# Kernel tuning notes

Hardware: AMD Instinct MI355X
Metric: run time of the kernel (lower is better)

Reference implementation:

```python
import jax, jax.numpy as jnp
import numpy as np

EMB = 384
NH = 6
HD = EMB // NH
EPS = 1e-5


def _ln(x, w, b):
    m = jnp.mean(x, axis=-1, keepdims=True)
    v = jnp.mean((x - m) ** 2, axis=-1, keepdims=True)
    return (x - m) * jax.lax.rsqrt(v + EPS) * w + b


def setup_inputs() -> dict:
    key = jax.random.key(0)
    ks = jax.random.split(key, 24)
    s = 0.02
    d = {
        "x": jax.random.normal(ks[0], (4, 4096, EMB), jnp.float32),
        "cond": jax.random.normal(ks[1], (4, EMB), jnp.float32),
        # AdaLN projections (weight stored as (in,out), bias (out,))
        "g1_w": jax.random.normal(ks[2], (EMB, EMB)) * s, "g1_b": jnp.zeros((EMB,)),
        "be1_w": jax.random.normal(ks[3], (EMB, EMB)) * s, "be1_b": jnp.zeros((EMB,)),
        "a1_w": jax.random.normal(ks[4], (EMB, EMB)) * s, "a1_b": jnp.zeros((EMB,)),
        "g2_w": jax.random.normal(ks[5], (EMB, EMB)) * s, "g2_b": jnp.zeros((EMB,)),
        "be2_w": jax.random.normal(ks[6], (EMB, EMB)) * s, "be2_b": jnp.zeros((EMB,)),
        "a2_w": jax.random.normal(ks[7], (EMB, EMB)) * s, "a2_b": jnp.zeros((EMB,)),
        "ln1_w": jnp.ones((EMB,)), "ln1_b": jnp.zeros((EMB,)),
        "ln2_w": jnp.ones((EMB,)), "ln2_b": jnp.zeros((EMB,)),
        "wq": jax.random.normal(ks[8], (EMB, EMB)) * s,
        "wk": jax.random.normal(ks[9], (EMB, EMB)) * s,
        "wv": jax.random.normal(ks[10], (EMB, EMB)) * s,
        "wo": jax.random.normal(ks[11], (EMB, EMB)) * s,
        "ff1_w": jax.random.normal(ks[12], (EMB, 4 * EMB)) * s, "ff1_b": jnp.zeros((4 * EMB,)),
        "ff2_w": jax.random.normal(ks[13], (4 * EMB, EMB)) * s, "ff2_b": jnp.zeros((EMB,)),
    }
    return d


def reference(x, cond,
              g1_w, g1_b, be1_w, be1_b, a1_w, a1_b,
              g2_w, g2_b, be2_w, be2_b, a2_w, a2_b,
              ln1_w, ln1_b, ln2_w, ln2_b,
              wq, wk, wv, wo,
              ff1_w, ff1_b, ff2_w, ff2_b):
    B, S, E = x.shape
    # AdaLN conditioning projections: (B, E)
    gamma1 = cond @ g1_w + g1_b
    beta1 = cond @ be1_w + be1_b
    alpha1 = cond @ a1_w + a1_b
    gamma2 = cond @ g2_w + g2_b
    beta2 = cond @ be2_w + be2_b
    alpha2 = cond @ a2_w + a2_b

    # Attention branch with AdaLN modulation
    y = _ln(x, ln1_w, ln1_b)
    y = y * (1.0 + gamma1[:, None, :]) + beta1[:, None, :]
    q = (y @ wq).reshape(B, S, NH, HD)
    k = (y @ wk).reshape(B, S, NH, HD)
    v = (y @ wv).reshape(B, S, NH, HD)
    scale = 1.0 / jnp.sqrt(jnp.array(HD, x.dtype))
    attn = jnp.einsum('bqhd,bkhd->bhqk', q, k) * scale  # [B,H,S,S]
    attn = jax.nn.softmax(attn, axis=-1)
    y = jnp.einsum('bhqk,bkhd->bqhd', attn, v).reshape(B, S, E)
    y = (y @ wo) * alpha1[:, None, :]
    y = x + y

    # FFN branch with AdaLN modulation
    z = _ln(y, ln2_w, ln2_b)
    z = z * (1.0 + gamma2[:, None, :]) + beta2[:, None, :]
    z = jax.nn.relu(z @ ff1_w + ff1_b) @ ff2_w + ff2_b
    z = z * alpha2[:, None, :]
    return y + z
```

## Files before the change

kernel.cpp:

```cpp
#include <hip/hip_runtime.h>
#include <stdint.h>

#define E 384
#define SEQ 4096
#define BATCH 4
#define NHEAD 6
#define HD 64
#define M_TOK 16384
#define QKVN 1152
#define FFH 1536

typedef __bf16 bf16x8 __attribute__((ext_vector_type(8)));
typedef __bf16 bf16x4 __attribute__((ext_vector_type(4)));
typedef float floatx4 __attribute__((ext_vector_type(4)));
typedef unsigned int uintx2 __attribute__((ext_vector_type(2)));
typedef unsigned int uintx4 __attribute__((ext_vector_type(4)));

__device__ __forceinline__ unsigned short f2b(float f) {
  unsigned int u = __builtin_bit_cast(unsigned int, f);
  u += 0x7fffu + ((u >> 16) & 1u);
  return (unsigned short)(u >> 16);
}

__device__ __forceinline__ void gl_lds16(const void* g, void* l) {
  __builtin_amdgcn_global_load_lds((__attribute__((address_space(1))) void*)g,
                                   (__attribute__((address_space(3))) void*)l,
                                   16, 0, 0);
}

__device__ __forceinline__ floatx4 mfma16(bf16x8 a, bf16x8 b, floatx4 c) {
  return __builtin_amdgcn_mfma_f32_16x16x32_bf16(a, b, c, 0, 0, 0);
}

__global__ __launch_bounds__(256) void prep_weights(
    const float* __restrict__ wq, const float* __restrict__ wk,
    const float* __restrict__ wv, const float* __restrict__ wo,
    const float* __restrict__ f1, const float* __restrict__ f2,
    unsigned short* __restrict__ qkv_t, unsigned short* __restrict__ wo_t,
    unsigned short* __restrict__ f1_t, unsigned short* __restrict__ f2_t) {
  int tid = blockIdx.x * 256 + threadIdx.x;
  const int R0 = QKVN * E;
  const int R1 = E * E;
  const int R2 = FFH * E;
  if (tid < R0) {
    int n = tid / E, k = tid - n * E;
    float v = (n < E) ? wq[k * E + n] : (n < 2 * E) ? wk[k * E + n - E] : wv[k * E + n - 2 * E];
    qkv_t[tid] = f2b(v);
  } else if (tid < R0 + R1) {
    int id = tid - R0;
    int n = id / E, k = id - n * E;
    wo_t[id] = f2b(wo[k * E + n]);
  } else if (tid < R0 + R1 + R2) {
    int id = tid - (R0 + R1);
    int n = id / E, k = id - n * E;
    f1_t[id] = f2b(f1[k * FFH + n]);
  } else {
    int id = tid - (R0 + R1 + R2);
    int n = id / FFH, k = id - n * FFH;
    f2_t[id] = f2b(f2[k * E + n]);
  }
}

__global__ __launch_bounds__(256) void cond_proj(
    const float* __restrict__ cond,
    const float* __restrict__ w0, const float* __restrict__ b0,
    const float* __restrict__ w1, const float* __restrict__ b1,
    const float* __restrict__ w2, const float* __restrict__ b2,
    const float* __restrict__ w3, const float* __restrict__ b3,
    const float* __restrict__ w4, const float* __restrict__ b4,
    const float* __restrict__ w5, const float* __restrict__ b5,
    float* __restrict__ outp) {
  int tid = blockIdx.x * 256 + threadIdx.x;
  int j = tid / (BATCH * E);
  int rem = tid - j * (BATCH * E);
  int b = rem / E, o = rem - b * E;
  const float* w; const float* bb;
  switch (j) {
    case 0: w = w0; bb = b0; break;
    case 1: w = w1; bb = b1; break;
    case 2: w = w2; bb = b2; break;
    case 3: w = w3; bb = b3; break;
    case 4: w = w4; bb = b4; break;
    default: w = w5; bb = b5; break;
  }
  float acc = bb[o];
  const float* c = cond + b * E;
  for (int i = 0; i < E; i++) acc += c[i] * w[i * E + o];
  outp[tid] = acc;
}

__global__ __launch_bounds__(256) void ln_mod(
    const float* __restrict__ in, const float* __restrict__ lw,
    const float* __restrict__ lb, const float* __restrict__ gamma,
    const float* __restrict__ beta, unsigned short* __restrict__ outb) {
  int lane = threadIdx.x & 63, wave = threadIdx.x >> 6;
  int m = blockIdx.x * 4 + wave;
  int b = m >> 12;
  const float* row = in + (size_t)m * E;
  float v[6], s = 0.f, s2 = 0.f;
#pragma unroll
  for (int i = 0; i < 6; i++) {
    float xv = row[lane + i * 64];
    v[i] = xv; s += xv; s2 += xv * xv;
  }
#pragma unroll
  for (int off = 32; off; off >>= 1) {
    s += __shfl_xor(s, off, 64);
    s2 += __shfl_xor(s2, off, 64);
  }
  float mean = s * (1.f / E);
  float var = s2 * (1.f / E) - mean * mean;
  float inv = rsqrtf(var + 1e-5f);
#pragma unroll
  for (int i = 0; i < 6; i++) {
    int e = lane + i * 64;
    float y = (v[i] - mean) * inv * lw[e] + lb[e];
    float g = gamma[b * E + e], be = beta[b * E + e];
    outb[(size_t)m * E + e] = f2b(y * (1.f + g) + be);
  }
}

template <int EPI>
__global__ __launch_bounds__(256) void gemm_bt(
    const unsigned short* __restrict__ A, const unsigned short* __restrict__ Bt,
    const float* __restrict__ bias, const float* __restrict__ alpha,
    const float* __restrict__ resid, float* __restrict__ outf,
    unsigned short* __restrict__ outb, int N, int K) {
  __shared__ __align__(16) unsigned short As[128 * 32];
  __shared__ __align__(16) unsigned short Bs[128 * 32];
  int t = threadIdx.x, lane = t & 63, wave = t >> 6;
  int m0 = blockIdx.y * 128, n0 = blockIdx.x * 128;
  int m15 = lane & 15, quad = lane >> 4;

  floatx4 acc[4][4];
  floatx4 vz = {0.f, 0.f, 0.f, 0.f};
#pragma unroll
  for (int i = 0; i < 4; i++)
#pragma unroll
    for (int j = 0; j < 4; j++) acc[i][j] = vz;

  int wm = (wave >> 1) * 64, wn = (wave & 1) * 64;
  int gsw = (quad ^ (m15 & 3)) * 8;

  for (int k0 = 0; k0 < K; k0 += 32) {
#pragma unroll
    for (int c = 0; c < 2; c++) {
      int t2 = c * 256 + t;
      int r = t2 >> 2;
      int G = (t2 & 3) ^ (r & 3);
      gl_lds16(A + (size_t)(m0 + r) * K + k0 + G * 8, As + (size_t)(c * 256 + wave * 64) * 8);
      gl_lds16(Bt + (size_t)(n0 + r) * K + k0 + G * 8, Bs + (size_t)(c * 256 + wave * 64) * 8);
    }
    __syncthreads();
    bf16x8 af[4], bf[4];
#pragma unroll
    for (int i = 0; i < 4; i++) {
      af[i] = *(const bf16x8*)&As[(wm + i * 16 + m15) * 32 + gsw];
      bf[i] = *(const bf16x8*)&Bs[(wn + i * 16 + m15) * 32 + gsw];
    }
#pragma unroll
    for (int mi = 0; mi < 4; mi++)
#pragma unroll
      for (int ni = 0; ni < 4; ni++) acc[mi][ni] = mfma16(af[mi], bf[ni], acc[mi][ni]);
    __syncthreads();
  }

  int rbase = quad * 4;
#pragma unroll
  for (int mi = 0; mi < 4; mi++) {
#pragma unroll
    for (int ni = 0; ni < 4; ni++) {
#pragma unroll
      for (int r = 0; r < 4; r++) {
        int row = m0 + wm + mi * 16 + rbase + r;
        int col = n0 + wn + ni * 16 + m15;
        float v = acc[mi][ni][r];
        if (EPI == 0) {
          outb[(size_t)row * N + col] = f2b(v);
        } else if (EPI == 1) {
          int b = row >> 12;
          size_t o = (size_t)row * E + col;
          outf[o] = resid[o] + v * alpha[b * E + col];
        } else if (EPI == 2) {
          v += bias[col];
          outb[(size_t)row * N + col] = f2b(v > 0.f ? v : 0.f);
        } else {
          int b = row >> 12;
          size_t o = (size_t)row * E + col;
          outf[o] = outf[o] + (v + bias[col]) * alpha[b * E + col];
        }
      }
    }
  }
}

template <int EPI>
__global__ __launch_bounds__(256) void gemm64(
    const unsigned short* __restrict__ A, const unsigned short* __restrict__ Bt,
    const float* __restrict__ bias, const float* __restrict__ alpha,
    const float* __restrict__ resid, float* __restrict__ outf,
    unsigned short* __restrict__ outb, int N, int K) {
  __shared__ __align__(16) unsigned short As[64 * 32];
  __shared__ __align__(16) unsigned short Bs[128 * 32];
  int t = threadIdx.x, lane = t & 63, wave = t >> 6;
  int m0 = blockIdx.y * 64, n0 = blockIdx.x * 128;
  int m15 = lane & 15, quad = lane >> 4;

  floatx4 acc[4][2];
  floatx4 vz = {0.f, 0.f, 0.f, 0.f};
#pragma unroll
  for (int i = 0; i < 4; i++)
#pragma unroll
    for (int j = 0; j < 2; j++) acc[i][j] = vz;

  int wn = wave * 32;
  int gsw = (quad ^ (m15 & 3)) * 8;

  for (int k0 = 0; k0 < K; k0 += 32) {
    {
      int r = t >> 2;
      int G = (t & 3) ^ (r & 3);
      gl_lds16(A + (size_t)(m0 + r) * K + k0 + G * 8, As + (size_t)(wave * 64) * 8);
    }
#pragma unroll
    for (int c = 0; c < 2; c++) {
      int t2 = c * 256 + t;
      int r = t2 >> 2;
      int G = (t2 & 3) ^ (r & 3);
      gl_lds16(Bt + (size_t)(n0 + r) * K + k0 + G * 8, Bs + (size_t)(c * 256 + wave * 64) * 8);
    }
    __syncthreads();
    bf16x8 af[4], bf[2];
#pragma unroll
    for (int i = 0; i < 4; i++) af[i] = *(const bf16x8*)&As[(i * 16 + m15) * 32 + gsw];
#pragma unroll
    for (int j = 0; j < 2; j++) bf[j] = *(const bf16x8*)&Bs[(wn + j * 16 + m15) * 32 + gsw];
#pragma unroll
    for (int mi = 0; mi < 4; mi++)
#pragma unroll
      for (int ni = 0; ni < 2; ni++) acc[mi][ni] = mfma16(af[mi], bf[ni], acc[mi][ni]);
    __syncthreads();
  }

  int rbase = quad * 4;
#pragma unroll
  for (int mi = 0; mi < 4; mi++) {
#pragma unroll
    for (int ni = 0; ni < 2; ni++) {
#pragma unroll
      for (int r = 0; r < 4; r++) {
        int row = m0 + mi * 16 + rbase + r;
        int col = n0 + wn + ni * 16 + m15;
        float v = acc[mi][ni][r];
        if (EPI == 1) {
          int b = row >> 12;
          size_t o = (size_t)row * E + col;
          outf[o] = resid[o] + v * alpha[b * E + col];
        } else {
          int b = row >> 12;
          size_t o = (size_t)row * E + col;
          outf[o] = outf[o] + (v + bias[col]) * alpha[b * E + col];
        }
      }
    }
  }
}

__global__ __launch_bounds__(256) void flash_attn(const unsigned short* __restrict__ qkv,
                                                  unsigned short* __restrict__ outb) {
  __shared__ __align__(16) unsigned short Qs[128 * 64];
  __shared__ __align__(16) unsigned short Ks[2][64 * 64];
  __shared__ __align__(16) unsigned short Vt[2][64 * 64];
  int t = threadIdx.x, lane = t & 63, wave = t >> 6;
  int m15 = lane & 15, quad = lane >> 4;
  int q0 = blockIdx.x * 128;
  int bh = blockIdx.y;
  int b = bh / NHEAD, h = bh - b * NHEAD;
  const unsigned short* qp = qkv + (size_t)b * SEQ * QKVN + h * HD;
  const unsigned short* kp = qp + E;
  const unsigned short* vp = qp + 2 * E;
  int kpr = t & 31, dg = t >> 5;

#pragma unroll
  for (int c = 0; c < 4; c++) {
    int slot = c * 256 + t;
    int qr = slot >> 3, s = slot & 7;
    int g = s ^ (qr & 7);
    gl_lds16(qp + (size_t)(q0 + qr) * QKVN + g * 8, Qs + (size_t)(c * 256 + wave * 64) * 8);
  }

  auto stageK = [&](int kb0, unsigned short* Kbuf) {
#pragma unroll
    for (int c = 0; c < 2; c++) {
      int slot = c * 256 + t;
      int kr = slot >> 3, s = slot & 7;
      int g = s ^ (kr & 7);
      gl_lds16(kp + (size_t)(kb0 + kr) * QKVN + g * 8, Kbuf + (size_t)(c * 256 + wave * 64) * 8);
    }
  };
  auto loadV = [&](int kb0, int4& r0, int4& r1) {
    r0 = *(const int4*)(vp + (size_t)(kb0 + 2 * kpr) * QKVN + dg * 8);
    r1 = *(const int4*)(vp + (size_t)(kb0 + 2 * kpr + 1) * QKVN + dg * 8);
  };
  auto writeVt = [&](unsigned short* Vbuf, int4 r0, int4 r1) {
    const unsigned short* u0 = (const unsigned short*)&r0;
    const unsigned short* u1 = (const unsigned short*)&r1;
    int kg = kpr >> 2, pos = kpr & 3;
    unsigned int* V32 = (unsigned int*)Vbuf;
#pragma unroll
    for (int i = 0; i < 8; i++) {
      int d = dg * 8 + i;
      V32[d * 32 + ((kg ^ i ^ dg) & 7) * 4 + pos] =
          (unsigned int)u0[i] | ((unsigned int)u1[i] << 16);
    }
  };

  stageK(0, Ks[0]);
  int4 va, vb;
  loadV(0, va, vb);
  writeVt(Vt[0], va, vb);
  __syncthreads();

  const float QSCALE = 0.125f * 1.44269504f;
  bf16x8 qf[2][2];
#pragma unroll
  for (int mt = 0; mt < 2; mt++) {
    int qr = wave * 32 + mt * 16 + m15;
#pragma unroll
    for (int dh = 0; dh < 2; dh++) {
      bf16x8 v = *(const bf16x8*)&Qs[qr * 64 + (((dh * 4 + quad) ^ (m15 & 7)) * 8)];
#pragma unroll
      for (int i = 0; i < 8; i++) v[i] = (__bf16)((float)v[i] * QSCALE);
      qf[mt][dh] = v;
    }
  }

  float lsum[2] = {0.f, 0.f};
  floatx4 of[2][4];
  floatx4 vz = {0.f, 0.f, 0.f, 0.f};
#pragma unroll
  for (int mt = 0; mt < 2; mt++)
#pragma unroll
    for (int dt = 0; dt < 4; dt++) of[mt][dt] = vz;

  int buf = 0;
  for (int kb0 = 0; kb0 < SEQ; kb0 += 64) {
    bf16x8 kf[4][2], vf[4][2];
#pragma unroll
    for (int kt = 0; kt < 4; kt++)
#pragma unroll
      for (int dh = 0; dh < 2; dh++)
        kf[kt][dh] =
            *(const bf16x8*)&Ks[buf][(kt * 16 + m15) * 64 + (((dh * 4 + quad) ^ (m15 & 7)) * 8)];
#pragma unroll
    for (int dt = 0; dt < 4; dt++)
#pragma unroll
      for (int kc = 0; kc < 2; kc++) {
        int d7 = m15 & 7, d3 = dt * 2 + (m15 >> 3);
        vf[dt][kc] = *(const bf16x8*)&Vt[buf][(dt * 16 + m15) * 64 +
                                             ((((kc * 4 + quad) ^ d7 ^ d3) & 7) * 8)];
      }

    int nkb = (kb0 + 64) & (SEQ - 1);
    stageK(nkb, Ks[buf ^ 1]);
    loadV(nkb, va, vb);

#pragma unroll
    for (int mt = 0; mt < 2; mt++) {
      floatx4 st[4];
#pragma unroll
      for (int kt = 0; kt < 4; kt++) {
        st[kt] = vz;
#pragma unroll
        for (int dh = 0; dh < 2; dh++) st[kt] = mfma16(kf[kt][dh], qf[mt][dh], st[kt]);
      }
      uintx2 pk[4];
      float lp = 0.f;
#pragma unroll
      for (int kt = 0; kt < 4; kt++) {
        floatx4 p;
#pragma unroll
        for (int r = 0; r < 4; r++) {
          p[r] = __builtin_amdgcn_exp2f(st[kt][r]);
          lp += p[r];
        }
        bf16x4 pb = __builtin_convertvector(p, bf16x4);
        pk[kt] = __builtin_bit_cast(uintx2, pb);
      }
      lsum[mt] += lp;

      int L0 = ((quad & 1) << 5) + m15;
      bool hi = (quad >> 1) != 0;
#pragma unroll
      for (int kc = 0; kc < 2; kc++) {
        int a0 = __shfl((int)pk[kc * 2].x, L0, 64);
        int a1 = __shfl((int)pk[kc * 2].y, L0, 64);
        int a2 = __shfl((int)pk[kc * 2].x, L0 + 16, 64);
        int a3 = __shfl((int)pk[kc * 2].y, L0 + 16, 64);
        int b0 = __shfl((int)pk[kc * 2 + 1].x, L0, 64);
        int b1 = __shfl((int)pk[kc * 2 + 1].y, L0, 64);
        int b2 = __shfl((int)pk[kc * 2 + 1].x, L0 + 16, 64);
        int b3 = __shfl((int)pk[kc * 2 + 1].y, L0 + 16, 64);
        uintx4 sel;
        sel.x = (unsigned)(hi ? b0 : a0);
        sel.y = (unsigned)(hi ? b1 : a1);
        sel.z = (unsigned)(hi ? b2 : a2);
        sel.w = (unsigned)(hi ? b3 : a3);
        bf16x8 pB = __builtin_bit_cast(bf16x8, sel);
#pragma unroll
        for (int dt = 0; dt < 4; dt++) of[mt][dt] = mfma16(vf[dt][kc], pB, of[mt][dt]);
      }
    }

    writeVt(Vt[buf ^ 1], va, vb);
    __syncthreads();
    buf ^= 1;
  }

#pragma unroll
  for (int mt = 0; mt < 2; mt++) {
    lsum[mt] += __shfl_xor(lsum[mt], 16, 64);
    lsum[mt] += __shfl_xor(lsum[mt], 32, 64);
    float inv = 1.f / lsum[mt];
    int q = q0 + wave * 32 + mt * 16 + m15;
    unsigned short* orow = outb + (size_t)(b * SEQ + q) * E + h * HD;
#pragma unroll
    for (int dt = 0; dt < 4; dt++) {
      floatx4 o;
#pragma unroll
      for (int r = 0; r < 4; r++) o[r] = of[mt][dt][r] * inv;
      bf16x4 ob = __builtin_convertvector(o, bf16x4);
      *(uintx2*)&orow[dt * 16 + quad * 4] = __builtin_bit_cast(uintx2, ob);
    }
  }
}

extern "C" void kernel_launch(void* const* d_in, const int* in_sizes, int n_in,
                              void* d_out, int out_size, void* d_ws, size_t ws_size,
                              hipStream_t stream) {
  const float* x     = (const float*)d_in[0];
  const float* cond  = (const float*)d_in[1];
  const float* g1_w  = (const float*)d_in[2];  const float* g1_b  = (const float*)d_in[3];
  const float* be1_w = (const float*)d_in[4];  const float* be1_b = (const float*)d_in[5];
  const float* a1_w  = (const float*)d_in[6];  const float* a1_b  = (const float*)d_in[7];
  const float* g2_w  = (const float*)d_in[8];  const float* g2_b  = (const float*)d_in[9];
  const float* be2_w = (const float*)d_in[10]; const float* be2_b = (const float*)d_in[11];
  const float* a2_w  = (const float*)d_in[12]; const float* a2_b  = (const float*)d_in[13];
  const float* ln1_w = (const float*)d_in[14]; const float* ln1_b = (const float*)d_in[15];
  const float* ln2_w = (const float*)d_in[16]; const float* ln2_b = (const float*)d_in[17];
  const float* wq    = (const float*)d_in[18]; const float* wk    = (const float*)d_in[19];
  const float* wv    = (const float*)d_in[20]; const float* wo    = (const float*)d_in[21];
  const float* ff1_w = (const float*)d_in[22]; const float* ff1_b = (const float*)d_in[23];
  const float* ff2_w = (const float*)d_in[24]; const float* ff2_b = (const float*)d_in[25];
  float* out = (float*)d_out;

  char* ws = (char*)d_ws;
  size_t off = 0;
  auto alloc = [&](size_t bytes) -> void* {
    void* p = ws + off;
    off += (bytes + 255) & ~(size_t)255;
    return p;
  };
  float* condp            = (float*)alloc((size_t)6 * BATCH * E * 4);
  unsigned short* wqkv_t  = (unsigned short*)alloc((size_t)QKVN * E * 2);
  unsigned short* wo_t    = (unsigned short*)alloc((size_t)E * E * 2);
  unsigned short* ff1_t   = (unsigned short*)alloc((size_t)FFH * E * 2);
  unsigned short* ff2_t   = (unsigned short*)alloc((size_t)E * FFH * 2);
  unsigned short* ymod    = (unsigned short*)alloc((size_t)M_TOK * E * 2);
  unsigned short* qkvbuf  = (unsigned short*)alloc((size_t)M_TOK * QKVN * 2);
  unsigned short* attnout = (unsigned short*)alloc((size_t)M_TOK * E * 2);
  unsigned short* hbuf    = (unsigned short*)alloc((size_t)M_TOK * FFH * 2);

  float* gamma1 = condp;            float* beta1 = condp + 1536;
  float* alpha1 = condp + 3072;     float* gamma2 = condp + 4608;
  float* beta2 = condp + 6144;      float* alpha2 = condp + 7680;

  prep_weights<<<6912, 256, 0, stream>>>(wq, wk, wv, wo, ff1_w, ff2_w,
                                         wqkv_t, wo_t, ff1_t, ff2_t);
  cond_proj<<<36, 256, 0, stream>>>(cond, g1_w, g1_b, be1_w, be1_b, a1_w, a1_b,
                                    g2_w, g2_b, be2_w, be2_b, a2_w, a2_b, condp);
  ln_mod<<<4096, 256, 0, stream>>>(x, ln1_w, ln1_b, gamma1, beta1, ymod);
  gemm_bt<0><<<dim3(QKVN / 128, M_TOK / 128), 256, 0, stream>>>(
      ymod, wqkv_t, nullptr, nullptr, nullptr, nullptr, qkvbuf, QKVN, E);
  flash_attn<<<dim3(SEQ / 128, BATCH * NHEAD), 256, 0, stream>>>(qkvbuf, attnout);
  gemm64<1><<<dim3(E / 128, M_TOK / 64), 256, 0, stream>>>(
      attnout, wo_t, nullptr, alpha1, x, out, nullptr, E, E);
  ln_mod<<<4096, 256, 0, stream>>>(out, ln2_w, ln2_b, gamma2, beta2, ymod);
  gemm_bt<2><<<dim3(FFH / 128, M_TOK / 128), 256, 0, stream>>>(
      ymod, ff1_t, ff1_b, nullptr, nullptr, nullptr, hbuf, FFH, E);
  gemm64<3><<<dim3(E / 128, M_TOK / 64), 256, 0, stream>>>(
      hbuf, ff2_t, ff2_b, alpha2, nullptr, out, nullptr, E, FFH);
}
```

Measured before the change: 466.4 us.

## Double-buffer LDS tiles in GEMMs and split-K the conditioning projection

Both GEMM kernels now keep two LDS buffers. The global-to-LDS loads for the next K-step are issued before the MFMAs on the current step, so load latency overlaps compute and each iteration needs one barrier instead of two. Separately, cond_proj splits its 384-long dot product into four chunks across four times as many blocks and combines them with atomicAdd. The output buffer is zeroed inside prep_weights for this. The cost is doubled LDS per GEMM block, which may lower occupancy, plus float atomics whose summation order is nondeterministic.

```diff
diff --git a/kernel.cpp b/kernel.cpp
--- a/kernel.cpp
+++ b/kernel.cpp
@@ -37,11 +37,13 @@
     const float* __restrict__ wv, const float* __restrict__ wo,
     const float* __restrict__ f1, const float* __restrict__ f2,
     unsigned short* __restrict__ qkv_t, unsigned short* __restrict__ wo_t,
-    unsigned short* __restrict__ f1_t, unsigned short* __restrict__ f2_t) {
+    unsigned short* __restrict__ f1_t, unsigned short* __restrict__ f2_t,
+    float* __restrict__ condp) {
   int tid = blockIdx.x * 256 + threadIdx.x;
   const int R0 = QKVN * E;
   const int R1 = E * E;
   const int R2 = FFH * E;
+  if (tid < 6 * BATCH * E) condp[tid] = 0.f;
   if (tid < R0) {
     int n = tid / E, k = tid - n * E;
     float v = (n < E) ? wq[k * E + n] : (n < 2 * E) ? wk[k * E + n - E] : wv[k * E + n - 2 * E];
@@ -71,8 +73,10 @@
     const float* __restrict__ w5, const float* __restrict__ b5,
     float* __restrict__ outp) {
   int tid = blockIdx.x * 256 + threadIdx.x;
-  int j = tid / (BATCH * E);
-  int rem = tid - j * (BATCH * E);
+  int id = tid % (6 * BATCH * E);
+  int ks = tid / (6 * BATCH * E);
+  int j = id / (BATCH * E);
+  int rem = id - j * (BATCH * E);
   int b = rem / E, o = rem - b * E;
   const float* w; const float* bb;
   switch (j) {
@@ -83,10 +87,11 @@
     case 4: w = w4; bb = b4; break;
     default: w = w5; bb = b5; break;
   }
-  float acc = bb[o];
+  float acc = (ks == 0) ? bb[o] : 0.f;
   const float* c = cond + b * E;
-  for (int i = 0; i < E; i++) acc += c[i] * w[i * E + o];
-  outp[tid] = acc;
+#pragma unroll 8
+  for (int i = ks * 96; i < ks * 96 + 96; i++) acc += c[i] * w[i * E + o];
+  atomicAdd(&outp[id], acc);
 }
 
 __global__ __launch_bounds__(256) void ln_mod(
@@ -126,8 +131,8 @@
     const float* __restrict__ bias, const float* __restrict__ alpha,
     const float* __restrict__ resid, float* __restrict__ outf,
     unsigned short* __restrict__ outb, int N, int K) {
-  __shared__ __align__(16) unsigned short As[128 * 32];
-  __shared__ __align__(16) unsigned short Bs[128 * 32];
+  __shared__ __align__(16) unsigned short As[2][128 * 32];
+  __shared__ __align__(16) unsigned short Bs[2][128 * 32];
   int t = threadIdx.x, lane = t & 63, wave = t >> 6;
   int m0 = blockIdx.y * 128, n0 = blockIdx.x * 128;
   int m15 = lane & 15, quad = lane >> 4;
@@ -142,21 +147,29 @@
   int wm = (wave >> 1) * 64, wn = (wave & 1) * 64;
   int gsw = (quad ^ (m15 & 3)) * 8;
 
-  for (int k0 = 0; k0 < K; k0 += 32) {
+  auto stage = [&](int k0, int sb) {
 #pragma unroll
     for (int c = 0; c < 2; c++) {
       int t2 = c * 256 + t;
       int r = t2 >> 2;
       int G = (t2 & 3) ^ (r & 3);
-      gl_lds16(A + (size_t)(m0 + r) * K + k0 + G * 8, As + (size_t)(c * 256 + wave * 64) * 8);
-      gl_lds16(Bt + (size_t)(n0 + r) * K + k0 + G * 8, Bs + (size_t)(c * 256 + wave * 64) * 8);
-    }
-    __syncthreads();
+      gl_lds16(A + (size_t)(m0 + r) * K + k0 + G * 8, &As[sb][(size_t)(c * 256 + wave * 64) * 8]);
+      gl_lds16(Bt + (size_t)(n0 + r) * K + k0 + G * 8, &Bs[sb][(size_t)(c * 256 + wave * 64) * 8]);
+    }
+  };
+
+  stage(0, 0);
+  __syncthreads();
+
+  int nsteps = K >> 5;
+  for (int s = 0; s < nsteps; s++) {
+    int cur = s & 1;
+    if (s + 1 < nsteps) stage((s + 1) << 5, cur ^ 1);
     bf16x8 af[4], bf[4];
 #pragma unroll
     for (int i = 0; i < 4; i++) {
-      af[i] = *(const bf16x8*)&As[(wm + i * 16 + m15) * 32 + gsw];
-      bf[i] = *(const bf16x8*)&Bs[(wn + i * 16 + m15) * 32 + gsw];
+      af[i] = *(const bf16x8*)&As[cur][(wm + i * 16 + m15) * 32 + gsw];
+      bf[i] = *(const bf16x8*)&Bs[cur][(wn + i * 16 + m15) * 32 + gsw];
     }
 #pragma unroll
     for (int mi = 0; mi < 4; mi++)
@@ -200,8 +213,8 @@
     const float* __restrict__ bias, const float* __restrict__ alpha,
     const float* __restrict__ resid, float* __restrict__ outf,
     unsigned short* __restrict__ outb, int N, int K) {
-  __shared__ __align__(16) unsigned short As[64 * 32];
-  __shared__ __align__(16) unsigned short Bs[128 * 32];
+  __shared__ __align__(16) unsigned short As[2][64 * 32];
+  __shared__ __align__(16) unsigned short Bs[2][128 * 32];
   int t = threadIdx.x, lane = t & 63, wave = t >> 6;
   int m0 = blockIdx.y * 64, n0 = blockIdx.x * 128;
   int m15 = lane & 15, quad = lane >> 4;
@@ -216,25 +229,33 @@
   int wn = wave * 32;
   int gsw = (quad ^ (m15 & 3)) * 8;
 
-  for (int k0 = 0; k0 < K; k0 += 32) {
+  auto stage = [&](int k0, int sb) {
     {
       int r = t >> 2;
       int G = (t & 3) ^ (r & 3);
-      gl_lds16(A + (size_t)(m0 + r) * K + k0 + G * 8, As + (size_t)(wave * 64) * 8);
+      gl_lds16(A + (size_t)(m0 + r) * K + k0 + G * 8, &As[sb][(size_t)(wave * 64) * 8]);
     }
 #pragma unroll
     for (int c = 0; c < 2; c++) {
       int t2 = c * 256 + t;
       int r = t2 >> 2;
       int G = (t2 & 3) ^ (r & 3);
-      gl_lds16(Bt + (size_t)(n0 + r) * K + k0 + G * 8, Bs + (size_t)(c * 256 + wave * 64) * 8);
-    }
-    __syncthreads();
+      gl_lds16(Bt + (size_t)(n0 + r) * K + k0 + G * 8, &Bs[sb][(size_t)(c * 256 + wave * 64) * 8]);
+    }
+  };
+
+  stage(0, 0);
+  __syncthreads();
+
+  int nsteps = K >> 5;
+  for (int s = 0; s < nsteps; s++) {
+    int cur = s & 1;
+    if (s + 1 < nsteps) stage((s + 1) << 5, cur ^ 1);
     bf16x8 af[4], bf[2];
 #pragma unroll
-    for (int i = 0; i < 4; i++) af[i] = *(const bf16x8*)&As[(i * 16 + m15) * 32 + gsw];
-#pragma unroll
-    for (int j = 0; j < 2; j++) bf[j] = *(const bf16x8*)&Bs[(wn + j * 16 + m15) * 32 + gsw];
+    for (int i = 0; i < 4; i++) af[i] = *(const bf16x8*)&As[cur][(i * 16 + m15) * 32 + gsw];
+#pragma unroll
+    for (int j = 0; j < 2; j++) bf[j] = *(const bf16x8*)&Bs[cur][(wn + j * 16 + m15) * 32 + gsw];
 #pragma unroll
     for (int mi = 0; mi < 4; mi++)
 #pragma unroll
@@ -476,9 +497,9 @@
   float* beta2 = condp + 6144;      float* alpha2 = condp + 7680;
 
   prep_weights<<<6912, 256, 0, stream>>>(wq, wk, wv, wo, ff1_w, ff2_w,
-                                         wqkv_t, wo_t, ff1_t, ff2_t);
-  cond_proj<<<36, 256, 0, stream>>>(cond, g1_w, g1_b, be1_w, be1_b, a1_w, a1_b,
-                                    g2_w, g2_b, be2_w, be2_b, a2_w, a2_b, condp);
+                                         wqkv_t, wo_t, ff1_t, ff2_t, condp);
+  cond_proj<<<144, 256, 0, stream>>>(cond, g1_w, g1_b, be1_w, be1_b, a1_w, a1_b,
+                                     g2_w, g2_b, be2_w, be2_b, a2_w, a2_b, condp);
   ln_mod<<<4096, 256, 0, stream>>>(x, ln1_w, ln1_b, gamma1, beta1, ymod);
   gemm_bt<0><<<dim3(QKVN / 128, M_TOK / 128), 256, 0, stream>>>(
       ymod, wqkv_t, nullptr, nullptr, nullptr, nullptr, qkvbuf, QKVN, E);
```

Result: faster. 450.4 us (-3.4%).
